# Kernel tuning notes

Hardware: AMD Instinct MI355X
Metric: run time of the kernel (lower is better)

Reference implementation:

```python
import jax, jax.numpy as jnp
from jax import lax
import numpy as np

N_QUBITS = 8
Q_DEPTH = 10
DIM = 256  # 2**8

# basis-state bit table; wire 0 = most-significant bit (PennyLane convention)
_bits = ((np.arange(DIM)[:, None] >> (N_QUBITS - 1 - np.arange(N_QUBITS))) & 1)
# phase layer: S on even wires (phase i), T on odd wires (phase e^{i pi/4})
_ph = np.where(np.arange(N_QUBITS) % 2 == 0, 1j, np.exp(1j * np.pi / 4))
_diag = np.prod(np.power(_ph[None, :], _bits), axis=1)
# entangling_layer_3 CZ pattern
_cz = np.ones(DIM)
for i, j in [(0, 1), (2, 3), (4, 5), (6, 7), (1, 2), (3, 4), (5, 6)]:
    _cz = _cz * ((-1.0) ** (_bits[:, i] * _bits[:, j]))
DIAG = jnp.asarray((_diag * _cz).astype(np.complex64))  # phase+CZ layer fused diagonal
ZSIGNS = jnp.asarray((1 - 2 * _bits).astype(np.float32))  # [256, 8] PauliZ eigenvalues
H_GATE = jnp.asarray((np.array([[1.0, 1.0], [1.0, -1.0]]) / np.sqrt(2.0)).astype(np.complex64))
X_GATE = jnp.asarray(np.array([[0.0, 1.0], [1.0, 0.0]]).astype(np.complex64))
EYE2 = jnp.eye(2, dtype=jnp.complex64)
BN_EPS = 1e-5


def apply_1q(state, U, w):
    """Apply 2x2 gate U on wire w; state: [B, 2,2,...,2]."""
    state = jnp.moveaxis(state, w + 1, -1)
    state = jnp.matmul(state, U.T)
    return jnp.moveaxis(state, -1, w + 1)


def quantum_net(features, q_params):
    """Batched statevector sim of quantum_net_3. features [B,256], q_params [80] -> [B,8]."""
    f = features / jnp.linalg.norm(features, axis=1, keepdims=True)
    state = f.astype(jnp.complex64).reshape((-1,) + (2,) * N_QUBITS)
    for w in range(N_QUBITS):
        state = apply_1q(state, H_GATE, w)
    qw = q_params.reshape(Q_DEPTH, N_QUBITS)
    for layer in range(Q_DEPTH):
        for w in range(N_QUBITS):
            t = qw[layer, w]
            c = jnp.cos(t / 2).astype(jnp.complex64)
            s = jnp.sin(t / 2).astype(jnp.complex64)
            U = c * EYE2 + (-1j) * s * X_GATE  # RX(t)
            state = apply_1q(state, U, w)
        flat = state.reshape(-1, DIM) * DIAG  # phase layer + CZ entangling (diagonal)
        state = flat.reshape((-1,) + (2,) * N_QUBITS)
    sv = state.reshape(-1, DIM)
    probs = sv.real ** 2 + sv.imag ** 2
    return probs @ ZSIGNS  # [B, 8] expval(PauliZ_i)


def conv2d(x, w, b):
    y = lax.conv_general_dilated(x, w, (1, 1), 'SAME', dimension_numbers=('NCHW', 'OIHW', 'NCHW'))
    return y + b[None, :, None, None]


def bn(x, gamma, beta, mean, var):  # eval-mode BatchNorm2d
    inv = gamma / jnp.sqrt(var + BN_EPS)
    return x * inv[None, :, None, None] + (beta - mean * inv)[None, :, None, None]


def maxpool2(x):
    return lax.reduce_window(x, -jnp.inf, lax.max, (1, 1, 2, 2), (1, 1, 2, 2), 'VALID')


def setup_inputs() -> dict:
    key = jax.random.key(0)
    ks = jax.random.split(key, 16)
    B = 1024
    return {
        'x': jax.random.normal(ks[0], (B, 1, 28, 28), dtype=jnp.float32),
        'conv1_w': 0.1 * jax.random.normal(ks[1], (32, 1, 3, 3), dtype=jnp.float32),
        'conv1_b': jnp.zeros((32,), jnp.float32),
        'bn1_gamma': jnp.ones((32,), jnp.float32),
        'bn1_beta': jnp.zeros((32,), jnp.float32),
        'bn1_mean': jnp.zeros((32,), jnp.float32),
        'bn1_var': jnp.ones((32,), jnp.float32),
        'conv2_w': 0.05 * jax.random.normal(ks[2], (64, 32, 3, 3), dtype=jnp.float32),
        'conv2_b': jnp.zeros((64,), jnp.float32),
        'bn2_gamma': jnp.ones((64,), jnp.float32),
        'bn2_beta': jnp.zeros((64,), jnp.float32),
        'bn2_mean': jnp.zeros((64,), jnp.float32),
        'bn2_var': jnp.ones((64,), jnp.float32),
        'fc_w': 0.01 * jax.random.normal(ks[3], (256, 64 * 7 * 7), dtype=jnp.float32),
        'fc_b': jnp.zeros((256,), jnp.float32),
        'q_params': 0.1 * jax.random.normal(ks[4], (Q_DEPTH * N_QUBITS,), dtype=jnp.float32),
        'p1_w': 0.01 * jax.random.normal(ks[5], (128, 8), dtype=jnp.float32),
        'p1_b': jnp.zeros((128,), jnp.float32),
        'p2_w': 0.01 * jax.random.normal(ks[6], (64, 128), dtype=jnp.float32),
        'p2_b': jnp.zeros((64,), jnp.float32),
        'p3_w': 0.01 * jax.random.normal(ks[7], (10, 64), dtype=jnp.float32),
        'p3_b': jnp.zeros((10,), jnp.float32),
    }


def reference(x, conv1_w, conv1_b, bn1_gamma, bn1_beta, bn1_mean, bn1_var,
              conv2_w, conv2_b, bn2_gamma, bn2_beta, bn2_mean, bn2_var,
              fc_w, fc_b, q_params, p1_w, p1_b, p2_w, p2_b, p3_w, p3_b):
    h = maxpool2(jax.nn.relu(bn(conv2d(x, conv1_w, conv1_b), bn1_gamma, bn1_beta, bn1_mean, bn1_var)))
    h = maxpool2(jax.nn.relu(bn(conv2d(h, conv2_w, conv2_b), bn2_gamma, bn2_beta, bn2_mean, bn2_var)))
    h = h.reshape(h.shape[0], -1)  # [B, 64*7*7]
    feats = jnp.tanh(h @ fc_w.T + fc_b)  # [B, 256]
    q = quantum_net(feats, q_params)  # [B, 8]
    z = jax.nn.relu(q @ p1_w.T + p1_b)  # dropout = identity (eval)
    z = jax.nn.relu(z @ p2_w.T + p2_b)
    return z @ p3_w.T + p3_b
```

## Files before the change

### kernel.cpp

```cpp
#include <hip/hip_runtime.h>
#include <math.h>


#define B_SZ 1024

#define OFF_FCWP   0
#define OFF_W2F    802816
#define OFF_W1T    821248
#define OFF_SC1    821536
#define OFF_SH1    821568
#define OFF_SC2    821600
#define OFF_SH2    821664
#define OFF_H1     821728
#define OFF_H2P    7244256

#define KSPLIT 7
#define KCHUNK 448

typedef __attribute__((ext_vector_type(8))) short s16x8;
typedef __attribute__((ext_vector_type(4))) float f32x4;

__constant__ float C_COS8[8] = {1.f, 0.70710678f, 0.f, -0.70710678f, -1.f, -0.70710678f, 0.f, 0.70710678f};
__constant__ float C_SIN8[8] = {0.f, 0.70710678f, 1.f, 0.70710678f, 0.f, -0.70710678f, -1.f, -0.70710678f};

__device__ __forceinline__ unsigned short bf16_rne(float f) {
  unsigned u = __float_as_uint(f);
  unsigned r = u + 0x7FFFu + ((u >> 16) & 1u);
  return (unsigned short)(r >> 16);
}
__device__ __forceinline__ int div14(int m) {
  return __float2int_rz((float)m * 0.07142858f);
}

__global__ __launch_bounds__(256) void prep_kernel(
    const float* __restrict__ fc_w, const float* __restrict__ c2w, const float* __restrict__ c1w,
    const float* __restrict__ bn1g, const float* __restrict__ bn1b, const float* __restrict__ bn1m,
    const float* __restrict__ bn1v, const float* __restrict__ c1b,
    const float* __restrict__ bn2g, const float* __restrict__ bn2b, const float* __restrict__ bn2m,
    const float* __restrict__ bn2v, const float* __restrict__ c2b,
    float* __restrict__ ws) {
  int g = blockIdx.x * 256 + threadIdx.x;
  int kp = g >> 8;
  int o  = g & 255;
  int s  = kp >> 6;
  int oc = kp & 63;
  ws[OFF_FCWP + kp * 256 + o] = fc_w[o * 3136 + oc * 49 + s];

  if (g < 36864) {
    int j = g & 7, L = (g >> 3) & 63, rest = g >> 9;
    int h = rest & 1; rest >>= 1;
    int t = rest % 9, w = rest / 9;
    int occ = w * 16 + (L & 15);
    int ic  = (L >> 4) * 8 + j;
    float v = c2w[occ * 288 + ic * 9 + t];
    unsigned short hi = bf16_rne(v);
    unsigned short res = hi;
    if (h) res = bf16_rne(v - __uint_as_float((unsigned)hi << 16));
    ((unsigned short*)(ws + OFF_W2F))[g] = res;
  }
  if (g < 288) {
    ws[OFF_W1T + g] = c1w[(g & 31) * 9 + (g >> 5)];
  }
  if (g < 32) {
    float inv = bn1g[g] / sqrtf(bn1v[g] + 1e-5f);
    ws[OFF_SC1 + g] = inv;
    ws[OFF_SH1 + g] = c1b[g] * inv + bn1b[g] - bn1m[g] * inv;
  }
  if (g < 64) {
    float inv = bn2g[g] / sqrtf(bn2v[g] + 1e-5f);
    ws[OFF_SC2 + g] = inv;
    ws[OFF_SH2 + g] = c2b[g] * inv + bn2b[g] - bn2m[g] * inv;
  }
}

__global__ __launch_bounds__(256) void conv1_kernel(
    const float* __restrict__ x, const float* __restrict__ w1T,
    const float* __restrict__ sc1, const float* __restrict__ sh1,
    float* __restrict__ h1) {
  const int b = blockIdx.x, tid = threadIdx.x;
  __shared__ float xs[30][32];
  __shared__ float w1s[288];
  __shared__ float sc1s[32], sh1s[32];

  float4* xsf = (float4*)&xs[0][0];
  if (tid < 240) xsf[tid] = make_float4(0.f, 0.f, 0.f, 0.f);
  __syncthreads();
  const float* xb = x + b * 784;
  for (int i = tid; i < 784; i += 256) {
    int y = i / 28, c = i - y * 28;
    xs[y + 1][c + 1] = xb[i];
  }
  for (int i = tid; i < 288; i += 256) w1s[i] = w1T[i];
  if (tid < 32) { sc1s[tid] = sc1[tid]; sh1s[tid] = sh1[tid]; }
  __syncthreads();

  for (int t = tid; t < 448; t += 256) {
    const int oc = t & 31, py = t >> 5;
    float wv[9];
#pragma unroll
    for (int k = 0; k < 9; ++k) wv[k] = w1s[k * 32 + oc];
    float acc0[28], acc1[28];
#pragma unroll
    for (int j = 0; j < 28; ++j) { acc0[j] = 0.f; acc1[j] = 0.f; }
#pragma unroll
    for (int r = 0; r < 4; ++r) {
      const int pr = 2 * py + r;
      float row[32];
#pragma unroll
      for (int q = 0; q < 8; ++q) {
        float4 v = *(const float4*)&xs[pr][4 * q];
        row[4 * q] = v.x; row[4 * q + 1] = v.y; row[4 * q + 2] = v.z; row[4 * q + 3] = v.w;
      }
      if (r <= 2) {
#pragma unroll
        for (int kx = 0; kx < 3; ++kx) {
          const float w = wv[r * 3 + kx];
#pragma unroll
          for (int xx = 0; xx < 28; ++xx) acc0[xx] = fmaf(row[xx + kx], w, acc0[xx]);
        }
      }
      if (r >= 1) {
#pragma unroll
        for (int kx = 0; kx < 3; ++kx) {
          const float w = wv[(r - 1) * 3 + kx];
#pragma unroll
          for (int xx = 0; xx < 28; ++xx) acc1[xx] = fmaf(row[xx + kx], w, acc1[xx]);
        }
      }
    }
    const float sc = sc1s[oc], sh = sh1s[oc];
    float* dst = h1 + b * 6272 + oc * 196 + py * 14;
#pragma unroll
    for (int px = 0; px < 14; ++px) {
      float v0 = fmaxf(fmaf(acc0[2 * px], sc, sh), 0.f);
      float v1 = fmaxf(fmaf(acc0[2 * px + 1], sc, sh), 0.f);
      float v2 = fmaxf(fmaf(acc1[2 * px], sc, sh), 0.f);
      float v3 = fmaxf(fmaf(acc1[2 * px + 1], sc, sh), 0.f);
      dst[px] = fmaxf(fmaxf(v0, v1), fmaxf(v2, v3));
    }
  }
}

__global__ __launch_bounds__(256, 2) void conv2_kernel(
    const float* __restrict__ h1, const float* __restrict__ w2f_f,
    const float* __restrict__ sc2, const float* __restrict__ sh2,
    float* __restrict__ h2p) {
  const int b = blockIdx.x, tid = threadIdx.x;
  const int lane = tid & 63, w = tid >> 6;

  __shared__ unsigned char lds_raw[50176];
  unsigned short* tile_hi = (unsigned short*)lds_raw;
  unsigned short* tile_lo = (unsigned short*)(lds_raw + 17408);
  float* conv_out = (float*)lds_raw;

  const unsigned short* w2f = (const unsigned short*)w2f_f;
  s16x8 bf[9][2];
#pragma unroll
  for (int t = 0; t < 9; ++t)
#pragma unroll
    for (int h = 0; h < 2; ++h)
      bf[t][h] = *(const s16x8*)&w2f[(((w * 9 + t) * 2 + h) << 9) + lane * 8];

  {
    float4* z = (float4*)lds_raw;
    for (int i = tid; i < 2176; i += 256) z[i] = make_float4(0.f, 0.f, 0.f, 0.f);
  }
  __syncthreads();

  if (tid < 196) {
    const int y = div14(tid), x = tid - y * 14;
    const int sp = ((y + 1) * 16 + (x + 1)) * 32;
    const float* src = h1 + b * 6272 + tid;
#pragma unroll
    for (int c = 0; c < 4; ++c) {
      s16x8 hv, lv;
#pragma unroll
      for (int j = 0; j < 8; ++j) {
        float v = src[(c * 8 + j) * 196];
        unsigned short h16 = bf16_rne(v);
        hv[j] = (short)h16;
        lv[j] = (short)bf16_rne(v - __uint_as_float((unsigned)h16 << 16));
      }
      *(s16x8*)&tile_hi[sp + c * 8] = hv;
      *(s16x8*)&tile_lo[sp + c * 8] = lv;
    }
  }
  __syncthreads();

  f32x4 acc[13];
#pragma unroll
  for (int i = 0; i < 13; ++i) acc[i] = (f32x4){0.f, 0.f, 0.f, 0.f};

  const int kg8 = (lane >> 4) * 8;
#pragma unroll
  for (int mt = 0; mt < 13; ++mt) {
    const int m = mt * 16 + (lane & 15);
    const int y = div14(m), x = m - y * 14;
    const int base = (y * 16 + x) * 32 + kg8;
#pragma unroll
    for (int dy = 0; dy < 3; ++dy) {
#pragma unroll
      for (int dx = 0; dx < 3; ++dx) {
        const int off = base + (dy * 16 + dx) * 32;
        s16x8 ah = *(s16x8*)&tile_hi[off];
        s16x8 al = *(s16x8*)&tile_lo[off];
        const int t = dy * 3 + dx;
        acc[mt] = __builtin_amdgcn_mfma_f32_16x16x32_bf16(ah, bf[t][0], acc[mt], 0, 0, 0);
        acc[mt] = __builtin_amdgcn_mfma_f32_16x16x32_bf16(ah, bf[t][1], acc[mt], 0, 0, 0);
        acc[mt] = __builtin_amdgcn_mfma_f32_16x16x32_bf16(al, bf[t][0], acc[mt], 0, 0, 0);
      }
    }
  }
  __syncthreads();

  const int oc = w * 16 + (lane & 15);
  const float sc = sc2[oc], sh = sh2[oc];
  float* cw = conv_out + w * 3136;
#pragma unroll
  for (int mt = 0; mt < 13; ++mt) {
#pragma unroll
    for (int r = 0; r < 4; ++r) {
      const int m = mt * 16 + (lane >> 4) * 4 + r;
      if (m < 196) cw[m * 16 + (lane & 15)] = fmaxf(fmaf(acc[mt][r], sc, sh), 0.f);
    }
  }
  __syncthreads();

#pragma unroll
  for (int i = 0; i < 13; ++i) {
    const int ps = i * 4 + (lane >> 4);
    if (ps < 49) {
      const int py = (ps * 37) >> 8, px = ps - py * 7;
      const int m00 = py * 28 + px * 2;
      const int c0 = m00 * 16 + (lane & 15);
      float v0 = cw[c0], v1 = cw[c0 + 16], v2 = cw[c0 + 224], v3 = cw[c0 + 240];
      h2p[b * 3136 + ps * 64 + oc] = fmaxf(fmaxf(v0, v1), fmaxf(v2, v3));
    }
  }
}

__global__ __launch_bounds__(256) void fc_kernel(
    const float* __restrict__ A, const float* __restrict__ Bp,
    float* __restrict__ Part) {
  __shared__ float As[32][34];
  __shared__ float Bs[32][68];
  const int tid = threadIdx.x;
  const int m0 = blockIdx.y * 32, n0 = blockIdx.x * 64;
  const int kbase = blockIdx.z * KCHUNK;
  const int am = tid >> 3, ak4 = tid & 7;
  const int bn4 = tid & 15, bk = tid >> 4;
  const int tx = tid & 15, ty = tid >> 4;
  float acc[2][4] = {{0.f, 0.f, 0.f, 0.f}, {0.f, 0.f, 0.f, 0.f}};
  for (int k0 = kbase; k0 < kbase + KCHUNK; k0 += 32) {
    float4 av  = *(const float4*)&A[(m0 + am) * 3136 + k0 + 4 * ak4];
    float4 bv0 = *(const float4*)&Bp[(k0 + bk) * 256 + n0 + 4 * bn4];
    float4 bv1 = *(const float4*)&Bp[(k0 + bk + 16) * 256 + n0 + 4 * bn4];
    As[4 * ak4 + 0][am] = av.x; As[4 * ak4 + 1][am] = av.y;
    As[4 * ak4 + 2][am] = av.z; As[4 * ak4 + 3][am] = av.w;
    *(float4*)&Bs[bk][4 * bn4] = bv0;
    *(float4*)&Bs[bk + 16][4 * bn4] = bv1;
    __syncthreads();
#pragma unroll
    for (int kk = 0; kk < 32; ++kk) {
      float2 a2 = *(const float2*)&As[kk][2 * ty];
      float4 b4 = *(const float4*)&Bs[kk][4 * tx];
      acc[0][0] = fmaf(a2.x, b4.x, acc[0][0]); acc[0][1] = fmaf(a2.x, b4.y, acc[0][1]);
      acc[0][2] = fmaf(a2.x, b4.z, acc[0][2]); acc[0][3] = fmaf(a2.x, b4.w, acc[0][3]);
      acc[1][0] = fmaf(a2.y, b4.x, acc[1][0]); acc[1][1] = fmaf(a2.y, b4.y, acc[1][1]);
      acc[1][2] = fmaf(a2.y, b4.z, acc[1][2]); acc[1][3] = fmaf(a2.y, b4.w, acc[1][3]);
    }
    __syncthreads();
  }
  float* dst = Part + blockIdx.z * 262144;
#pragma unroll
  for (int i = 0; i < 2; ++i) {
    const int m = m0 + 2 * ty + i;
    *(float4*)&dst[m * 256 + n0 + 4 * tx] =
        make_float4(acc[i][0], acc[i][1], acc[i][2], acc[i][3]);
  }
}

__global__ __launch_bounds__(256) void quantum_kernel(
    const float* __restrict__ Part, const float* __restrict__ fc_b,
    const float* __restrict__ qp,
    const float* __restrict__ p1w, const float* __restrict__ p1b,
    const float* __restrict__ p2w, const float* __restrict__ p2b,
    const float* __restrict__ p3w, const float* __restrict__ p3b,
    float* __restrict__ out) {
  const int b = blockIdx.x, tid = threadIdx.x;
  __shared__ float2 buf[2][256];
  __shared__ float csl[160];
  __shared__ float part[4][8];
  __shared__ float qv[8];
  __shared__ float z1[128];
  __shared__ float z2s[64];

  if (tid < 80) {
    float t = 0.5f * qp[tid];
    csl[2 * tid] = cosf(t);
    csl[2 * tid + 1] = sinf(t);
  }

  float f = fc_b[tid];
#pragma unroll
  for (int z = 0; z < KSPLIT; ++z) f += Part[z * 262144 + b * 256 + tid];
  f = tanhf(f);

  float ss = f * f;
#pragma unroll
  for (int off = 32; off >= 1; off >>= 1) ss += __shfl_xor(ss, off);
  const int lane = tid & 63, wid = tid >> 6;
  if (lane == 0) part[wid][0] = ss;
  __syncthreads();
  const float tot = part[0][0] + part[1][0] + part[2][0] + part[3][0];
  const float inv = 1.0f / sqrtf(tot);
  float re = f * inv, im = 0.f;

  const int k8 = (2 * __popc(tid & 0xAA) + __popc(tid & 0x55)) & 7;
  float dre = C_COS8[k8], dim_ = C_SIN8[k8];
  {
    const int i = tid;
    int par = ((i >> 7) & (i >> 6)) ^ ((i >> 5) & (i >> 4)) ^ ((i >> 3) & (i >> 2)) ^ ((i >> 1) & i)
            ^ ((i >> 6) & (i >> 5)) ^ ((i >> 4) & (i >> 3)) ^ ((i >> 2) & (i >> 1));
    if (par & 1) { dre = -dre; dim_ = -dim_; }
  }

  int cur = 0;
  const float RS = 0.70710678118654752f;

#pragma unroll
  for (int w = 0; w < 2; ++w) {
    const int m = 128 >> w;
    cur ^= 1;
    buf[cur][tid] = make_float2(re, im);
    __syncthreads();
    float2 p = buf[cur][tid ^ m];
    float sgn = (tid & m) ? -1.f : 1.f;
    re = fmaf(sgn, re, p.x) * RS;
    im = fmaf(sgn, im, p.y) * RS;
  }
#pragma unroll
  for (int w = 2; w < 8; ++w) {
    const int m = 1 << (7 - w);
    float pre = __shfl_xor(re, m);
    float pim = __shfl_xor(im, m);
    float sgn = (tid & m) ? -1.f : 1.f;
    re = fmaf(sgn, re, pre) * RS;
    im = fmaf(sgn, im, pim) * RS;
  }

  for (int layer = 0; layer < 10; ++layer) {
    const float* cs = &csl[16 * layer];
#pragma unroll
    for (int w = 0; w < 2; ++w) {
      const int m = 128 >> w;
      const float c = cs[2 * w], s = cs[2 * w + 1];
      cur ^= 1;
      buf[cur][tid] = make_float2(re, im);
      __syncthreads();
      float2 p = buf[cur][tid ^ m];
      float nre = fmaf(s, p.y, c * re);
      float nim = fmaf(-s, p.x, c * im);
      re = nre; im = nim;
    }
#pragma unroll
    for (int w = 2; w < 8; ++w) {
      const int m = 1 << (7 - w);
      const float c = cs[2 * w], s = cs[2 * w + 1];
      float pre = __shfl_xor(re, m);
      float pim = __shfl_xor(im, m);
      float nre = fmaf(s, pim, c * re);
      float nim = fmaf(-s, pre, c * im);
      if (w == 7) {
        float tre = nre * dre - nim * dim_;
        nim = fmaf(nre, dim_, nim * dre);
        nre = tre;
      }
      re = nre; im = nim;
    }
  }

  const float prb = re * re + im * im;
#pragma unroll
  for (int w = 0; w < 8; ++w) {
    float v = ((tid >> (7 - w)) & 1) ? -prb : prb;
#pragma unroll
    for (int off = 32; off >= 1; off >>= 1) v += __shfl_xor(v, off);
    if (lane == 0) part[wid][w] = v;
  }
  __syncthreads();
  if (tid < 8) qv[tid] = part[0][tid] + part[1][tid] + part[2][tid] + part[3][tid];
  __syncthreads();

  if (tid < 128) {
    float a = p1b[tid];
#pragma unroll
    for (int k = 0; k < 8; ++k) a = fmaf(qv[k], p1w[tid * 8 + k], a);
    z1[tid] = fmaxf(a, 0.f);
  }
  __syncthreads();
  if (tid < 64) {
    float a = p2b[tid];
#pragma unroll 16
    for (int k = 0; k < 128; ++k) a = fmaf(z1[k], p2w[tid * 128 + k], a);
    z2s[tid] = fmaxf(a, 0.f);
  }
  __syncthreads();
  if (tid < 10) {
    float a = p3b[tid];
#pragma unroll 16
    for (int k = 0; k < 64; ++k) a = fmaf(z2s[k], p3w[tid * 64 + k], a);
    out[b * 10 + tid] = a;
  }
}

extern "C" void kernel_launch(void* const* d_in, const int* in_sizes, int n_in,
                              void* d_out, int out_size, void* d_ws, size_t ws_size,
                              hipStream_t stream) {
  (void)in_sizes; (void)n_in; (void)out_size; (void)ws_size;
  const float* x    = (const float*)d_in[0];
  const float* c1w  = (const float*)d_in[1];
  const float* c1b  = (const float*)d_in[2];
  const float* bn1g = (const float*)d_in[3];
  const float* bn1b = (const float*)d_in[4];
  const float* bn1m = (const float*)d_in[5];
  const float* bn1v = (const float*)d_in[6];
  const float* c2w  = (const float*)d_in[7];
  const float* c2b  = (const float*)d_in[8];
  const float* bn2g = (const float*)d_in[9];
  const float* bn2b = (const float*)d_in[10];
  const float* bn2m = (const float*)d_in[11];
  const float* bn2v = (const float*)d_in[12];
  const float* fc_w = (const float*)d_in[13];
  const float* fc_b = (const float*)d_in[14];
  const float* qp   = (const float*)d_in[15];
  const float* p1w  = (const float*)d_in[16];
  const float* p1b  = (const float*)d_in[17];
  const float* p2w  = (const float*)d_in[18];
  const float* p2b  = (const float*)d_in[19];
  const float* p3w  = (const float*)d_in[20];
  const float* p3b  = (const float*)d_in[21];
  float* ws = (float*)d_ws;
  float* outp = (float*)d_out;

  prep_kernel<<<3136, 256, 0, stream>>>(fc_w, c2w, c1w,
                                        bn1g, bn1b, bn1m, bn1v, c1b,
                                        bn2g, bn2b, bn2m, bn2v, c2b, ws);
  conv1_kernel<<<B_SZ, 256, 0, stream>>>(x, ws + OFF_W1T, ws + OFF_SC1, ws + OFF_SH1, ws + OFF_H1);
  conv2_kernel<<<B_SZ, 256, 0, stream>>>(ws + OFF_H1, ws + OFF_W2F, ws + OFF_SC2, ws + OFF_SH2, ws + OFF_H2P);
  fc_kernel<<<dim3(4, 32, KSPLIT), 256, 0, stream>>>(ws + OFF_H2P, ws + OFF_FCWP, ws + OFF_H1);
  quantum_kernel<<<B_SZ, 256, 0, stream>>>(ws + OFF_H1, fc_b, qp, p1w, p1b, p2w, p2b, p3w, p3b, outp);
}
```

Before: 195.5 us.

## Replace FP32 FC GEMM with split-bf16 MFMA kernel and fragment-packed weights

The FC layer (1024x3136 by 3136x256) moves from a scalar FP32 LDS-tiled GEMM to a bf16 MFMA kernel. It uses a hi/lo split (three MFMAs per fragment) to keep close to FP32 accuracy. conv2 now writes its pooled activations as hi/lo bf16 pairs, and prep packs fc_w into MFMA B-fragment layout. The K split doubles to 14, which adds more partial sums for the quantum kernel to reduce. In exchange it cuts FP32 FMA work and halves activation traffic per copy.

```diff
diff --git a/kernel.cpp b/kernel.cpp
--- a/kernel.cpp
+++ b/kernel.cpp
@@ -14,8 +14,8 @@
 #define OFF_H1     821728
 #define OFF_H2P    7244256
 
-#define KSPLIT 7
-#define KCHUNK 448
+#define KSPLIT_FC 14
+#define KCHUNK_FC 224
 
 typedef __attribute__((ext_vector_type(8))) short s16x8;
 typedef __attribute__((ext_vector_type(4))) float f32x4;
@@ -40,11 +40,19 @@
     const float* __restrict__ bn2v, const float* __restrict__ c2b,
     float* __restrict__ ws) {
   int g = blockIdx.x * 256 + threadIdx.x;
-  int kp = g >> 8;
-  int o  = g & 255;
-  int s  = kp >> 6;
-  int oc = kp & 63;
-  ws[OFF_FCWP + kp * 256 + o] = fc_w[o * 3136 + oc * 49 + s];
+
+  {
+    int j = g & 7, lane = (g >> 3) & 63, nt = (g >> 9) & 15, kg = g >> 13;
+    int n = nt * 16 + (lane & 15);
+    int k = kg * 32 + ((lane >> 4) & 3) * 8 + j;
+    float v = fc_w[n * 3136 + (k & 63) * 49 + (k >> 6)];
+    unsigned short hi = bf16_rne(v);
+    unsigned short lo = bf16_rne(v - __uint_as_float((unsigned)hi << 16));
+    unsigned short* us = (unsigned short*)ws;
+    int base = ((kg * 16 + nt) * 2) * 512 + lane * 8 + j;
+    us[base] = hi;
+    us[base + 512] = lo;
+  }
 
   if (g < 36864) {
     int j = g & 7, L = (g >> 3) & 63, rest = g >> 9;
@@ -144,7 +152,7 @@
 __global__ __launch_bounds__(256, 2) void conv2_kernel(
     const float* __restrict__ h1, const float* __restrict__ w2f_f,
     const float* __restrict__ sc2, const float* __restrict__ sh2,
-    float* __restrict__ h2p) {
+    unsigned short* __restrict__ h2hi, unsigned short* __restrict__ h2lo) {
   const int b = blockIdx.x, tid = threadIdx.x;
   const int lane = tid & 63, w = tid >> 6;
 
@@ -234,49 +242,66 @@
       const int m00 = py * 28 + px * 2;
       const int c0 = m00 * 16 + (lane & 15);
       float v0 = cw[c0], v1 = cw[c0 + 16], v2 = cw[c0 + 224], v3 = cw[c0 + 240];
-      h2p[b * 3136 + ps * 64 + oc] = fmaxf(fmaxf(v0, v1), fmaxf(v2, v3));
-    }
-  }
-}
-
-__global__ __launch_bounds__(256) void fc_kernel(
-    const float* __restrict__ A, const float* __restrict__ Bp,
-    float* __restrict__ Part) {
-  __shared__ float As[32][34];
-  __shared__ float Bs[32][68];
+      float vm = fmaxf(fmaxf(v0, v1), fmaxf(v2, v3));
+      unsigned short hv = bf16_rne(vm);
+      const int idx = b * 3136 + ps * 64 + oc;
+      h2hi[idx] = hv;
+      h2lo[idx] = bf16_rne(vm - __uint_as_float((unsigned)hv << 16));
+    }
+  }
+}
+
+__global__ __launch_bounds__(256) void fc_mfma_kernel(
+    const unsigned short* __restrict__ h2hi, const unsigned short* __restrict__ h2lo,
+    const unsigned short* __restrict__ Bfrag, float* __restrict__ Part) {
+  __shared__ unsigned short Bs[8192];
   const int tid = threadIdx.x;
-  const int m0 = blockIdx.y * 32, n0 = blockIdx.x * 64;
-  const int kbase = blockIdx.z * KCHUNK;
-  const int am = tid >> 3, ak4 = tid & 7;
-  const int bn4 = tid & 15, bk = tid >> 4;
-  const int tx = tid & 15, ty = tid >> 4;
-  float acc[2][4] = {{0.f, 0.f, 0.f, 0.f}, {0.f, 0.f, 0.f, 0.f}};
-  for (int k0 = kbase; k0 < kbase + KCHUNK; k0 += 32) {
-    float4 av  = *(const float4*)&A[(m0 + am) * 3136 + k0 + 4 * ak4];
-    float4 bv0 = *(const float4*)&Bp[(k0 + bk) * 256 + n0 + 4 * bn4];
-    float4 bv1 = *(const float4*)&Bp[(k0 + bk + 16) * 256 + n0 + 4 * bn4];
-    As[4 * ak4 + 0][am] = av.x; As[4 * ak4 + 1][am] = av.y;
-    As[4 * ak4 + 2][am] = av.z; As[4 * ak4 + 3][am] = av.w;
-    *(float4*)&Bs[bk][4 * bn4] = bv0;
-    *(float4*)&Bs[bk + 16][4 * bn4] = bv1;
+  const int lane = tid & 63, w = tid >> 6;
+  const int m0 = blockIdx.y * 64, nt0 = blockIdx.x * 8, z = blockIdx.z;
+  const int kz = z * KCHUNK_FC;
+
+  const int mrow = m0 + w * 16 + (lane & 15);
+  const int kg8 = (lane >> 4) * 8;
+  const unsigned short* arow_hi = h2hi + mrow * 3136;
+  const unsigned short* arow_lo = h2lo + mrow * 3136;
+
+  f32x4 acc[8];
+#pragma unroll
+  for (int i = 0; i < 8; ++i) acc[i] = (f32x4){0.f, 0.f, 0.f, 0.f};
+
+  for (int c = 0; c < 7; ++c) {
+    const int kg = (kz >> 5) + c;
+    {
+      const uint4* src = (const uint4*)(Bfrag + (size_t)(kg * 16 + nt0) * 1024);
+      uint4* dst = (uint4*)Bs;
+#pragma unroll
+      for (int i = 0; i < 4; ++i) dst[tid + 256 * i] = src[tid + 256 * i];
+    }
     __syncthreads();
-#pragma unroll
-    for (int kk = 0; kk < 32; ++kk) {
-      float2 a2 = *(const float2*)&As[kk][2 * ty];
-      float4 b4 = *(const float4*)&Bs[kk][4 * tx];
-      acc[0][0] = fmaf(a2.x, b4.x, acc[0][0]); acc[0][1] = fmaf(a2.x, b4.y, acc[0][1]);
-      acc[0][2] = fmaf(a2.x, b4.z, acc[0][2]); acc[0][3] = fmaf(a2.x, b4.w, acc[0][3]);
-      acc[1][0] = fmaf(a2.y, b4.x, acc[1][0]); acc[1][1] = fmaf(a2.y, b4.y, acc[1][1]);
-      acc[1][2] = fmaf(a2.y, b4.z, acc[1][2]); acc[1][3] = fmaf(a2.y, b4.w, acc[1][3]);
+
+    const int k0 = kz + c * 32;
+    s16x8 ah = *(const s16x8*)(arow_hi + k0 + kg8);
+    s16x8 al = *(const s16x8*)(arow_lo + k0 + kg8);
+#pragma unroll
+    for (int nf = 0; nf < 8; ++nf) {
+      s16x8 bh = *(s16x8*)&Bs[(nf * 2 + 0) * 512 + lane * 8];
+      s16x8 bl = *(s16x8*)&Bs[(nf * 2 + 1) * 512 + lane * 8];
+      acc[nf] = __builtin_amdgcn_mfma_f32_16x16x32_bf16(ah, bh, acc[nf], 0, 0, 0);
+      acc[nf] = __builtin_amdgcn_mfma_f32_16x16x32_bf16(ah, bl, acc[nf], 0, 0, 0);
+      acc[nf] = __builtin_amdgcn_mfma_f32_16x16x32_bf16(al, bh, acc[nf], 0, 0, 0);
     }
     __syncthreads();
   }
-  float* dst = Part + blockIdx.z * 262144;
-#pragma unroll
-  for (int i = 0; i < 2; ++i) {
-    const int m = m0 + 2 * ty + i;
-    *(float4*)&dst[m * 256 + n0 + 4 * tx] =
-        make_float4(acc[i][0], acc[i][1], acc[i][2], acc[i][3]);
+
+  float* dst = Part + (size_t)z * 262144;
+  const int mbase = m0 + w * 16 + (lane >> 4) * 4;
+  const int nbase = nt0 * 16 + (lane & 15);
+#pragma unroll
+  for (int nf = 0; nf < 8; ++nf) {
+#pragma unroll
+    for (int r = 0; r < 4; ++r) {
+      dst[(mbase + r) * 256 + nbase + nf * 16] = acc[nf][r];
+    }
   }
 }
 
@@ -303,7 +328,7 @@
 
   float f = fc_b[tid];
 #pragma unroll
-  for (int z = 0; z < KSPLIT; ++z) f += Part[z * 262144 + b * 256 + tid];
+  for (int z = 0; z < KSPLIT_FC; ++z) f += Part[z * 262144 + b * 256 + tid];
   f = tanhf(f);
 
   float ss = f * f;
@@ -443,11 +468,16 @@
   float* ws = (float*)d_ws;
   float* outp = (float*)d_out;
 
+  unsigned short* h2hi = (unsigned short*)(ws + OFF_H2P);
+  unsigned short* h2lo = h2hi + 3211264;
+  const unsigned short* bfrag = (const unsigned short*)ws;
+
   prep_kernel<<<3136, 256, 0, stream>>>(fc_w, c2w, c1w,
                                         bn1g, bn1b, bn1m, bn1v, c1b,
                                         bn2g, bn2b, bn2m, bn2v, c2b, ws);
   conv1_kernel<<<B_SZ, 256, 0, stream>>>(x, ws + OFF_W1T, ws + OFF_SC1, ws + OFF_SH1, ws + OFF_H1);
-  conv2_kernel<<<B_SZ, 256, 0, stream>>>(ws + OFF_H1, ws + OFF_W2F, ws + OFF_SC2, ws + OFF_SH2, ws + OFF_H2P);
-  fc_kernel<<<dim3(4, 32, KSPLIT), 256, 0, stream>>>(ws + OFF_H2P, ws + OFF_FCWP, ws + OFF_H1);
+  conv2_kernel<<<B_SZ, 256, 0, stream>>>(ws + OFF_H1, ws + OFF_W2F, ws + OFF_SC2, ws + OFF_SH2,
+                                         h2hi, h2lo);
+  fc_mfma_kernel<<<dim3(2, 16, KSPLIT_FC), 256, 0, stream>>>(h2hi, h2lo, bfrag, ws + OFF_H1);
   quantum_kernel<<<B_SZ, 256, 0, stream>>>(ws + OFF_H1, fc_b, qp, p1w, p1b, p2w, p2b, p3w, p3b, outp);
 }
```

Result: faster. 177.6 us (-9.2%).
